# Performance work log

Hardware: AMD Instinct MI355X
Metric: run time of the kernel (lower is better)

The kernel has to match this reference:

```python
import jax, jax.numpy as jnp
import numpy as np

N, E, D, H = 100000, 200000, 384, 768
BN_EPS = 1e-5


def setup_inputs() -> dict:
    key = jax.random.key(0)
    ks = jax.random.split(key, 8)
    w = lambda k, sh: jax.random.normal(k, sh, jnp.float32) * 0.02
    return {
        "x": jax.random.normal(ks[0], (N, D), jnp.float32),
        "edge_attr": jax.random.normal(ks[1], (E, D), jnp.float32),
        "gamma": jnp.ones((D,), jnp.float32),
        "beta": jnp.zeros((D,), jnp.float32),
        "eps": jnp.zeros((), jnp.float32),          # GINE train_eps, init 0
        "W_edge": w(ks[2], (D, D)),
        "b_edge": jnp.zeros((D,), jnp.float32),
        "W1": w(ks[3], (D, H)),
        "b1": jnp.zeros((H,), jnp.float32),
        "W2": w(ks[4], (H, D)),
        "b2": jnp.zeros((D,), jnp.float32),
        "edge_index": jax.random.randint(ks[5], (2, E), 0, N, jnp.int32),
    }


def reference(x, edge_attr, gamma, beta, eps, W_edge, b_edge, W1, b1, W2, b2, edge_index):
    # BatchNorm1d over the node (batch) dimension, training statistics
    mu = jnp.mean(x, axis=0)
    var = jnp.var(x, axis=0)
    h = (x - mu) * jax.lax.rsqrt(var + BN_EPS) * gamma + beta  # [N, D]

    src, dst = edge_index[0], edge_index[1]  # j -> i (PyG source_to_target)
    # GINEConv message: relu(x_j + lin(edge_attr))
    msg = jax.nn.relu(h[src] + edge_attr @ W_edge + b_edge)     # [E, D]
    agg = jax.ops.segment_sum(msg, dst, num_segments=N)         # sum aggregation

    # nn((1+eps)*x_i + agg) where nn = Linear->GELU->Linear
    z = (1.0 + eps) * h + agg
    z = jax.nn.gelu(z @ W1 + b1, approximate=False) @ W2 + b2

    # residual + outer GELU activation (drop_path/dropout = identity at eval)
    return x + jax.nn.gelu(z, approximate=False)
```

## Files before the change

kernel.cpp:

```cpp
#include <hip/hip_runtime.h>
#include <hip/hip_bf16.h>

#define Df 384
#define Hf 768
#define SCAN_CH 4096

typedef __bf16 bf16x8 __attribute__((ext_vector_type(8)));
typedef float f32x4 __attribute__((ext_vector_type(4)));

struct __attribute__((aligned(4))) U12 { unsigned int x, y, z; };

__device__ inline unsigned short f2bf(float f) {
    __hip_bfloat16 h = __float2bfloat16(f);
    return __builtin_bit_cast(unsigned short, h);
}
__device__ inline float bf2f(unsigned short u) {
    unsigned int v = ((unsigned int)u) << 16;
    return __builtin_bit_cast(float, v);
}
__device__ inline float lobf(unsigned int v) { return bf2f((unsigned short)(v & 0xffff)); }
__device__ inline float hibf(unsigned int v) { return bf2f((unsigned short)(v >> 16)); }
__device__ inline unsigned int pk2(float a, float b) {
    return (unsigned int)f2bf(a) | ((unsigned int)f2bf(b) << 16);
}
__device__ inline float gelu_(float v) {
    return 0.5f * v * (1.0f + erff(v * 0.70710678118654752f));
}
__device__ inline void gload16(const void* g, void* l) {
    __builtin_amdgcn_global_load_lds(
        (const __attribute__((address_space(1))) unsigned int*)g,
        (__attribute__((address_space(3))) unsigned int*)l, 16, 0, 0);
}

__global__ void bn_stats(const float* __restrict__ x, float* __restrict__ stats, int N) {
    int t = threadIdx.x;
    int c4 = (t % 96) * 4;
    int rs = t / 96;
    float s0 = 0, s1 = 0, s2 = 0, s3 = 0, q0 = 0, q1 = 0, q2 = 0, q3 = 0;
    for (int r = blockIdx.x * 2 + rs; r < N; r += gridDim.x * 2) {
        float4 v = *(const float4*)(x + (size_t)r * Df + c4);
        s0 += v.x; s1 += v.y; s2 += v.z; s3 += v.w;
        q0 += v.x * v.x; q1 += v.y * v.y; q2 += v.z * v.z; q3 += v.w * v.w;
    }
    unsafeAtomicAdd(&stats[c4 + 0], s0);
    unsafeAtomicAdd(&stats[c4 + 1], s1);
    unsafeAtomicAdd(&stats[c4 + 2], s2);
    unsafeAtomicAdd(&stats[c4 + 3], s3);
    unsafeAtomicAdd(&stats[Df + c4 + 0], q0);
    unsafeAtomicAdd(&stats[Df + c4 + 1], q1);
    unsafeAtomicAdd(&stats[Df + c4 + 2], q2);
    unsafeAtomicAdd(&stats[Df + c4 + 3], q3);
}

__global__ void bn_finalize(const float* __restrict__ stats,
                            const float* __restrict__ gamma,
                            const float* __restrict__ beta,
                            float* __restrict__ coef, int N) {
    int c = threadIdx.x;
    float invN = 1.0f / (float)N;
    float mu = stats[c] * invN;
    float var = stats[Df + c] * invN - mu * mu;
    float rs = rsqrtf(var + 1e-5f);
    float a = gamma[c] * rs;
    coef[c] = a;
    coef[Df + c] = beta[c] - mu * a;
}

__global__ void h_kernel(const float* __restrict__ x, const float* __restrict__ coef,
                         unsigned short* __restrict__ hb, int tot8) {
    int i = blockIdx.x * 256 + threadIdx.x;
    if (i >= tot8) return;
    size_t base = (size_t)i * 8;
    int c = (int)(base % Df);
    float4 x0 = *(const float4*)(x + base);
    float4 x1 = *(const float4*)(x + base + 4);
    const float* a = coef + c;
    const float* b = coef + Df + c;
    uint4 o;
    o.x = pk2(x0.x * a[0] + b[0], x0.y * a[1] + b[1]);
    o.y = pk2(x0.z * a[2] + b[2], x0.w * a[3] + b[3]);
    o.z = pk2(x1.x * a[4] + b[4], x1.y * a[5] + b[5]);
    o.w = pk2(x1.z * a[6] + b[6], x1.w * a[7] + b[7]);
    *(uint4*)(hb + base) = o;
}

__global__ void wtrans(const float* __restrict__ Wsrc, unsigned short* __restrict__ Wdst,
                       int K, int Nc) {
    int idx = blockIdx.x * 256 + threadIdx.x;
    if (idx >= K * Nc) return;
    int k = idx / Nc, n = idx % Nc;
    Wdst[(size_t)n * K + k] = f2bf(Wsrc[idx]);
}

__global__ void degree_k(const int* __restrict__ dst, int* __restrict__ deg, int E) {
    int e = blockIdx.x * 256 + threadIdx.x;
    if (e < E) atomicAdd(&deg[dst[e]], 1);
}

__global__ void scan1(const int* __restrict__ deg, int* __restrict__ off,
                      int* __restrict__ sums, int N) {
    __shared__ int ts[256];
    int t = threadIdx.x;
    int base = blockIdx.x * SCAN_CH + t * 16;
    int v[16];
    int s = 0;
    for (int j = 0; j < 16; j++) {
        int idx = base + j;
        int d = (idx < N) ? deg[idx] : 0;
        v[j] = s;
        s += d;
    }
    ts[t] = s;
    __syncthreads();
    for (int o = 1; o < 256; o <<= 1) {
        int add = (t >= o) ? ts[t - o] : 0;
        __syncthreads();
        ts[t] += add;
        __syncthreads();
    }
    int pre = t ? ts[t - 1] : 0;
    for (int j = 0; j < 16; j++) {
        int idx = base + j;
        if (idx < N) off[idx] = pre + v[j];
    }
    if (t == 255) sums[blockIdx.x] = ts[255];
}

__global__ void scan2(int* __restrict__ sums, int nb) {
    int acc = 0;
    for (int b = 0; b < nb; b++) { int v = sums[b]; sums[b] = acc; acc += v; }
    sums[nb] = acc;
}

__global__ void scan3(int* __restrict__ off, const int* __restrict__ sums, int N, int nb) {
    int idx = blockIdx.x * 256 + threadIdx.x;
    if (idx < N) off[idx] += sums[idx / SCAN_CH];
    else if (idx == N) off[N] = sums[nb];
}

__global__ void fill_k(const int* __restrict__ dst, const int* __restrict__ src,
                       int* __restrict__ cursor, int* __restrict__ srcp,
                       int* __restrict__ pose, int E) {
    int e = blockIdx.x * 256 + threadIdx.x;
    if (e >= E) return;
    int pos = atomicAdd(&cursor[dst[e]], 1);
    srcp[pos] = src[e];
    pose[e] = pos;
}

__global__ __launch_bounds__(256) void aggregate(
    const unsigned short* __restrict__ msgl, const unsigned short* __restrict__ hb,
    const int* __restrict__ off, const int* __restrict__ srcp,
    const float* __restrict__ epsp,
    unsigned short* __restrict__ zb, int N) {
    int lane = threadIdx.x & 63;
    int wid = threadIdx.x >> 6;
    int nwaves = gridDim.x * 4;
    float s1p = 1.0f + epsp[0];
    int loff = lane * 6;
    for (int i = blockIdx.x * 4 + wid; i < N; i += nwaves) {
        int o0 = off[i], o1 = off[i + 1];
        float a0 = 0, a1 = 0, a2 = 0, a3 = 0, a4 = 0, a5 = 0;
        for (int p = o0; p < o1; ++p) {
            int s = srcp[p];
            U12 mv = *(const U12*)(msgl + (size_t)p * Df + loff);
            U12 hv = *(const U12*)(hb + (size_t)s * Df + loff);
            a0 += fmaxf(lobf(mv.x) + lobf(hv.x), 0.f);
            a1 += fmaxf(hibf(mv.x) + hibf(hv.x), 0.f);
            a2 += fmaxf(lobf(mv.y) + lobf(hv.y), 0.f);
            a3 += fmaxf(hibf(mv.y) + hibf(hv.y), 0.f);
            a4 += fmaxf(lobf(mv.z) + lobf(hv.z), 0.f);
            a5 += fmaxf(hibf(mv.z) + hibf(hv.z), 0.f);
        }
        U12 hv = *(const U12*)(hb + (size_t)i * Df + loff);
        U12 o;
        o.x = pk2(s1p * lobf(hv.x) + a0, s1p * hibf(hv.x) + a1);
        o.y = pk2(s1p * lobf(hv.y) + a2, s1p * hibf(hv.y) + a3);
        o.z = pk2(s1p * lobf(hv.z) + a4, s1p * hibf(hv.z) + a5);
        *(U12*)(zb + (size_t)i * Df + loff) = o;
    }
}

template <int EPI, bool ABF16>
__global__ __launch_bounds__(256) void gemm_fused(
    const void* __restrict__ Ap, const unsigned short* __restrict__ Bt,
    const float* __restrict__ bias, int M, int K, int ncols,
    const int* __restrict__ pose,
    unsigned short* __restrict__ outb,
    const float* __restrict__ xres, float* __restrict__ outf, int ldo) {
    __shared__ __align__(16) unsigned short As[2][128 * 32];
    __shared__ __align__(16) unsigned short Bs[2][128 * 32];
    const int t = threadIdx.x;
    const int nwg = gridDim.x;
    const int orig = blockIdx.x;
    const int xcd = orig & 7;
    const int q = nwg >> 3, r = nwg & 7;
    const int wgid = (xcd < r ? xcd * (q + 1) : r * (q + 1) + (xcd - r) * q) + (orig >> 3);
    const int pp = wgid / ncols;
    const int m0 = pp * 128;
    const int n0 = (wgid - pp * ncols) * 128;

    const int lane = t & 63;
    const int wid = t >> 6;
    const int wr = (wid >> 1) << 6;
    const int wc = (wid & 1) << 6;
    const int fr = lane & 15;
    const int kg = lane >> 4;
    const int crow = lane >> 2;
    const int cseg = lane & 3;
    const int sr = t >> 1;
    const int sh = (t & 1) << 4;

    f32x4 acc[4][4];
#pragma unroll
    for (int i = 0; i < 4; i++)
#pragma unroll
        for (int j = 0; j < 4; j++) acc[i][j] = (f32x4){0.f, 0.f, 0.f, 0.f};

    const bool arok = (m0 + sr) < M;
    const size_t arowoff = (size_t)(m0 + sr) * K;
    const int NT = K >> 5;

    auto stageB = [&](int buf, int k0) {
#pragma unroll
        for (int h = 0; h < 2; h++) {
            const int rbase = wid * 32 + h * 16;
            gload16(Bt + (size_t)(n0 + rbase + crow) * K + k0 + cseg * 8,
                    &Bs[buf][rbase * 32]);
        }
    };
    auto stageA16 = [&](int buf, int k0) {
        const unsigned short* Ab = (const unsigned short*)Ap;
#pragma unroll
        for (int h = 0; h < 2; h++) {
            const int rbase = wid * 32 + h * 16;
            if (m0 + rbase + crow < M)
                gload16(Ab + (size_t)(m0 + rbase + crow) * K + k0 + cseg * 8,
                        &As[buf][rbase * 32]);
        }
    };

    if (ABF16) {
        stageA16(0, 0);
    } else if (arok) {
        const float4* p = (const float4*)((const float*)Ap + arowoff + sh);
        float4 f0 = p[0], f1 = p[1], f2 = p[2], f3 = p[3];
        uint4 w0, w1;
        w0.x = pk2(f0.x, f0.y); w0.y = pk2(f0.z, f0.w);
        w0.z = pk2(f1.x, f1.y); w0.w = pk2(f1.z, f1.w);
        w1.x = pk2(f2.x, f2.y); w1.y = pk2(f2.z, f2.w);
        w1.z = pk2(f3.x, f3.y); w1.w = pk2(f3.z, f3.w);
        *(uint4*)&As[0][sr * 32 + sh] = w0;
        *(uint4*)&As[0][sr * 32 + sh + 8] = w1;
    }
    stageB(0, 0);
    __syncthreads();

    int cur = 0;
    for (int kt = 0; kt < NT; ++kt) {
        const int nxt = cur ^ 1;
        const bool more = (kt + 1) < NT;
        float4 f0, f1, f2, f3;
        if (more) {
            const int k0n = (kt + 1) * 32;
            if (ABF16) {
                stageA16(nxt, k0n);
            } else if (arok) {
                const float4* p = (const float4*)((const float*)Ap + arowoff + k0n + sh);
                f0 = p[0]; f1 = p[1]; f2 = p[2]; f3 = p[3];
            }
            stageB(nxt, k0n);
        }

        bf16x8 a[4], b[4];
#pragma unroll
        for (int i = 0; i < 4; i++) a[i] = *(const bf16x8*)&As[cur][(wr + i * 16 + fr) * 32 + kg * 8];
#pragma unroll
        for (int j = 0; j < 4; j++) b[j] = *(const bf16x8*)&Bs[cur][(wc + j * 16 + fr) * 32 + kg * 8];
#pragma unroll
        for (int i = 0; i < 4; i++)
#pragma unroll
            for (int j = 0; j < 4; j++)
                acc[i][j] = __builtin_amdgcn_mfma_f32_16x16x32_bf16(a[i], b[j], acc[i][j], 0, 0, 0);

        if (!ABF16 && more && arok) {
            uint4 w0, w1;
            w0.x = pk2(f0.x, f0.y); w0.y = pk2(f0.z, f0.w);
            w0.z = pk2(f1.x, f1.y); w0.w = pk2(f1.z, f1.w);
            w1.x = pk2(f2.x, f2.y); w1.y = pk2(f2.z, f2.w);
            w1.z = pk2(f3.x, f3.y); w1.w = pk2(f3.z, f3.w);
            *(uint4*)&As[nxt][sr * 32 + sh] = w0;
            *(uint4*)&As[nxt][sr * 32 + sh + 8] = w1;
        }
        __syncthreads();
        cur = nxt;
    }

    const int kg4 = kg * 4;
#pragma unroll
    for (int i = 0; i < 4; i++) {
        const int rb = m0 + wr + i * 16 + kg4;
#pragma unroll
        for (int j = 0; j < 4; j++) {
            const int c = n0 + wc + j * 16 + fr;
#pragma unroll
            for (int r = 0; r < 4; r++) {
                const int row = rb + r;
                if (row < M) {
                    float v = acc[i][j][r] + bias[c];
                    if (EPI == 1) {
                        outb[(size_t)row * ldo + c] = f2bf(gelu_(v));
                    } else if (EPI == 2) {
                        size_t o = (size_t)row * ldo + c;
                        outf[o] = xres[o] + gelu_(v);
                    } else {
                        outb[(size_t)pose[row] * ldo + c] = f2bf(v);
                    }
                }
            }
        }
    }
}

extern "C" void kernel_launch(void* const* d_in, const int* in_sizes, int n_in,
                              void* d_out, int out_size, void* d_ws, size_t ws_size,
                              hipStream_t stream) {
    const float* x = (const float*)d_in[0];
    const float* ea = (const float*)d_in[1];
    const float* gamma = (const float*)d_in[2];
    const float* beta = (const float*)d_in[3];
    const float* epsp = (const float*)d_in[4];
    const float* W_edge = (const float*)d_in[5];
    const float* b_edge = (const float*)d_in[6];
    const float* W1 = (const float*)d_in[7];
    const float* b1 = (const float*)d_in[8];
    const float* W2 = (const float*)d_in[9];
    const float* b2 = (const float*)d_in[10];
    const int* eidx = (const int*)d_in[11];
    float* out = (float*)d_out;
    const int N = in_sizes[0] / Df;
    const int E = in_sizes[1] / Df;
    const int* esrc = eidx;
    const int* edst = eidx + E;

    char* w = (char*)d_ws;
    size_t off_ = 0;
    auto alloc = [&](size_t bytes) { char* p = w + off_; off_ += (bytes + 255) & ~(size_t)255; return p; };
    float* stats = (float*)alloc(2 * Df * sizeof(float));
    float* coef = (float*)alloc(2 * Df * sizeof(float));
    unsigned short* hb = (unsigned short*)alloc((size_t)N * Df * 2);
    unsigned short* zb = (unsigned short*)alloc((size_t)N * Df * 2);
    unsigned short* tb = (unsigned short*)alloc((size_t)N * Hf * 2);
    unsigned short* WeT = (unsigned short*)alloc((size_t)Df * Df * 2);
    unsigned short* W1T = (unsigned short*)alloc((size_t)Df * Hf * 2);
    unsigned short* W2T = (unsigned short*)alloc((size_t)Hf * Df * 2);
    int* deg = (int*)alloc((size_t)(N + 1) * 4);
    int* offs = (int*)alloc((size_t)(N + 1) * 4);
    int* srcp = (int*)alloc((size_t)E * 4);
    int* pose = (int*)alloc((size_t)E * 4);
    int* sums = (int*)alloc(64 * 4);
    size_t msgl_bytes = (size_t)E * Df * 2;
    unsigned short* msgl;
    if (off_ + msgl_bytes <= ws_size) msgl = (unsigned short*)alloc(msgl_bytes);
    else msgl = (unsigned short*)d_out;
    (void)n_in; (void)out_size;

    hipMemsetAsync(stats, 0, 2 * Df * sizeof(float), stream);
    hipMemsetAsync(deg, 0, (size_t)N * 4, stream);

    bn_stats<<<1024, 192, 0, stream>>>(x, stats, N);
    bn_finalize<<<1, Df, 0, stream>>>(stats, gamma, beta, coef, N);
    int tot8 = N * Df / 8;
    h_kernel<<<(tot8 + 255) / 256, 256, 0, stream>>>(x, coef, hb, tot8);

    wtrans<<<(Df * Df + 255) / 256, 256, 0, stream>>>(W_edge, WeT, Df, Df);
    wtrans<<<(Df * Hf + 255) / 256, 256, 0, stream>>>(W1, W1T, Df, Hf);
    wtrans<<<(Hf * Df + 255) / 256, 256, 0, stream>>>(W2, W2T, Hf, Df);

    int nb = (N + SCAN_CH - 1) / SCAN_CH;
    degree_k<<<(E + 255) / 256, 256, 0, stream>>>(edst, deg, E);
    scan1<<<nb, 256, 0, stream>>>(deg, offs, sums, N);
    scan2<<<1, 1, 0, stream>>>(sums, nb);
    scan3<<<(N + 256) / 256, 256, 0, stream>>>(offs, sums, N, nb);
    hipMemcpyAsync(deg, offs, (size_t)N * 4, hipMemcpyDeviceToDevice, stream);
    fill_k<<<(E + 255) / 256, 256, 0, stream>>>(edst, esrc, deg, srcp, pose, E);

    int ep = (E + 127) / 128;
    gemm_fused<3, false><<<dim3(ep * (Df / 128)), 256, 0, stream>>>(
        ea, WeT, b_edge, E, Df, Df / 128, pose, msgl, nullptr, nullptr, Df);

    aggregate<<<2048, 256, 0, stream>>>(msgl, hb, offs, srcp, epsp, zb, N);

    int np = (N + 127) / 128;
    gemm_fused<1, true><<<dim3(np * (Hf / 128)), 256, 0, stream>>>(
        zb, W1T, b1, N, Df, Hf / 128, nullptr, tb, nullptr, nullptr, Hf);
    gemm_fused<2, true><<<dim3(np * (Df / 128)), 256, 0, stream>>>(
        tb, W2T, b2, N, Hf, Df / 128, nullptr, nullptr, x, out, Df);
}
```

Before: 1.085 ms.

## Add persistent B-stationary GEMM for first MLP layer and merge weight transposes

The first MLP GEMM (z @ W1 + GELU) now runs in a new persistent kernel. Each block loads a 64-column slice of W1 (the full K=384) into swizzled LDS once, then walks 128-row strips of the activations, reading A straight from global memory into MFMA registers with one step of prefetch. This removes the repeated B tile reloads and the double-buffered LDS staging of the generic GEMM. The three weight-transpose launches are also merged into one kernel to cut launch overhead. In exchange, the new kernel gives up A reuse through LDS, so each A row is read from global memory 12 times, once per column slice, and it depends on the XCD-to-strip mapping for L2 locality.

```diff
diff --git a/kernel.cpp b/kernel.cpp
--- a/kernel.cpp
+++ b/kernel.cpp
@@ -84,12 +84,23 @@
     *(uint4*)(hb + base) = o;
 }
 
-__global__ void wtrans(const float* __restrict__ Wsrc, unsigned short* __restrict__ Wdst,
-                       int K, int Nc) {
+__global__ void wtrans3(const float* __restrict__ We, const float* __restrict__ W1,
+                        const float* __restrict__ W2,
+                        unsigned short* __restrict__ WeT, unsigned short* __restrict__ W1T,
+                        unsigned short* __restrict__ W2T) {
     int idx = blockIdx.x * 256 + threadIdx.x;
-    if (idx >= K * Nc) return;
-    int k = idx / Nc, n = idx % Nc;
-    Wdst[(size_t)n * K + k] = f2bf(Wsrc[idx]);
+    if (idx < Df * Df) {
+        int k = idx / Df, n = idx % Df;
+        WeT[n * Df + k] = f2bf(We[idx]);
+    } else if (idx < Df * Df + Df * Hf) {
+        int i = idx - Df * Df;
+        int k = i / Hf, n = i % Hf;
+        W1T[(size_t)n * Df + k] = f2bf(W1[i]);
+    } else if (idx < Df * Df + 2 * Df * Hf) {
+        int i = idx - (Df * Df + Df * Hf);
+        int k = i / Df, n = i % Df;
+        W2T[(size_t)n * Hf + k] = f2bf(W2[i]);
+    }
 }
 
 __global__ void degree_k(const int* __restrict__ dst, int* __restrict__ deg, int E) {
@@ -181,6 +192,101 @@
     }
 }
 
+__global__ __launch_bounds__(256, 3) void gemm_ts(
+    const unsigned short* __restrict__ Ab,
+    const unsigned short* __restrict__ Bt,
+    const float* __restrict__ bias,
+    unsigned short* __restrict__ outb,
+    int M) {
+    __shared__ __align__(16) unsigned short Bs[64 * Df];
+
+    const int t = threadIdx.x;
+    const int lane = t & 63;
+    const int wid = t >> 6;
+    const int fr = lane & 15;
+    const int kg = lane >> 4;
+    const int orig = blockIdx.x;
+    const int xcd = orig & 7;
+    const int local = orig >> 3;
+    const int cs = local % 12;
+    const int rsub = local / 12;
+    const int cb = cs * 64;
+    const int first = xcd * 8 + rsub;
+    const int STRIPS = (M + 127) >> 7;
+
+#pragma unroll
+    for (int s = 0; s < 12; s++) {
+        int u = s * 256 + t;
+        int col = u / 48;
+        int pos = u - col * 48;
+        gload16(Bt + (size_t)(cb + col) * Df + ((pos ^ (col & 7)) << 3),
+                &Bs[(s * 256 + wid * 64) * 8]);
+    }
+    asm volatile("s_waitcnt vmcnt(0)" ::: "memory");
+    __builtin_amdgcn_s_barrier();
+
+    float bv[4];
+#pragma unroll
+    for (int j = 0; j < 4; j++) bv[j] = bias[cb + j * 16 + fr];
+
+    for (int s = first; s < STRIPS; s += 64) {
+        const int r0 = s * 128 + wid * 32;
+        int ra0 = r0 + fr;       if (ra0 >= M) ra0 = M - 1;
+        int ra1 = r0 + 16 + fr;  if (ra1 >= M) ra1 = M - 1;
+        const unsigned short* pA0 = Ab + (size_t)ra0 * Df + kg * 8;
+        const unsigned short* pA1 = Ab + (size_t)ra1 * Df + kg * 8;
+
+        f32x4 acc[2][4];
+#pragma unroll
+        for (int i = 0; i < 2; i++)
+#pragma unroll
+            for (int j = 0; j < 4; j++) acc[i][j] = (f32x4){0.f, 0.f, 0.f, 0.f};
+
+        uint4 a0 = *(const uint4*)(pA0);
+        uint4 a1 = *(const uint4*)(pA1);
+#pragma unroll
+        for (int kt = 0; kt < 12; kt++) {
+            uint4 n0, n1;
+            if (kt < 11) {
+                n0 = *(const uint4*)(pA0 + (kt + 1) * 32);
+                n1 = *(const uint4*)(pA1 + (kt + 1) * 32);
+            } else { n0 = a0; n1 = a1; }
+            bf16x8 bf[4];
+#pragma unroll
+            for (int j = 0; j < 4; j++) {
+                const int cl = j * 16 + fr;
+                const int unit = (kt * 4 + kg) ^ (cl & 7);
+                bf[j] = *(const bf16x8*)&Bs[(cl * 48 + unit) * 8];
+            }
+            bf16x8 av0 = __builtin_bit_cast(bf16x8, a0);
+            bf16x8 av1 = __builtin_bit_cast(bf16x8, a1);
+#pragma unroll
+            for (int j = 0; j < 4; j++) {
+                acc[0][j] = __builtin_amdgcn_mfma_f32_16x16x32_bf16(av0, bf[j], acc[0][j], 0, 0, 0);
+                acc[1][j] = __builtin_amdgcn_mfma_f32_16x16x32_bf16(av1, bf[j], acc[1][j], 0, 0, 0);
+            }
+            a0 = n0; a1 = n1;
+        }
+
+        const int kg4 = kg * 4;
+#pragma unroll
+        for (int i = 0; i < 2; i++) {
+            const int rb = r0 + i * 16 + kg4;
+#pragma unroll
+            for (int r = 0; r < 4; r++) {
+                const int row = rb + r;
+                if (row < M) {
+#pragma unroll
+                    for (int j = 0; j < 4; j++) {
+                        outb[(size_t)row * Hf + cb + j * 16 + fr] =
+                            f2bf(gelu_(acc[i][j][r] + bv[j]));
+                    }
+                }
+            }
+        }
+    }
+}
+
 template <int EPI, bool ABF16>
 __global__ __launch_bounds__(256) void gemm_fused(
     const void* __restrict__ Ap, const unsigned short* __restrict__ Bt,
@@ -308,9 +414,7 @@
                 const int row = rb + r;
                 if (row < M) {
                     float v = acc[i][j][r] + bias[c];
-                    if (EPI == 1) {
-                        outb[(size_t)row * ldo + c] = f2bf(gelu_(v));
-                    } else if (EPI == 2) {
+                    if (EPI == 2) {
                         size_t o = (size_t)row * ldo + c;
                         outf[o] = xres[o] + gelu_(v);
                     } else {
@@ -373,9 +477,8 @@
     int tot8 = N * Df / 8;
     h_kernel<<<(tot8 + 255) / 256, 256, 0, stream>>>(x, coef, hb, tot8);
 
-    wtrans<<<(Df * Df + 255) / 256, 256, 0, stream>>>(W_edge, WeT, Df, Df);
-    wtrans<<<(Df * Hf + 255) / 256, 256, 0, stream>>>(W1, W1T, Df, Hf);
-    wtrans<<<(Hf * Df + 255) / 256, 256, 0, stream>>>(W2, W2T, Hf, Df);
+    wtrans3<<<(Df * Df + 2 * Df * Hf + 255) / 256, 256, 0, stream>>>(
+        W_edge, W1, W2, WeT, W1T, W2T);
 
     int nb = (N + SCAN_CH - 1) / SCAN_CH;
     degree_k<<<(E + 255) / 256, 256, 0, stream>>>(edst, deg, E);
@@ -391,9 +494,9 @@
 
     aggregate<<<2048, 256, 0, stream>>>(msgl, hb, offs, srcp, epsp, zb, N);
 
+    gemm_ts<<<768, 256, 0, stream>>>(zb, W1T, b1, tb, N);
+
     int np = (N + 127) / 128;
-    gemm_fused<1, true><<<dim3(np * (Hf / 128)), 256, 0, stream>>>(
-        zb, W1T, b1, N, Df, Hf / 128, nullptr, tb, nullptr, nullptr, Hf);
     gemm_fused<2, true><<<dim3(np * (Df / 128)), 256, 0, stream>>>(
         tb, W2T, b2, N, Hf, Df / 128, nullptr, nullptr, x, out, Df);
 }
```

Result: slower. 1.146 ms (+5.7%).
